# Kernel optimization log

Measured on AMD Instinct MI355X. Metric: run time of the kernel, lower is better.

Reference implementation:

```python
import jax, jax.numpy as jnp
import numpy as np

D_MODEL = 1024
NUM_HEADS = 16
D_K = D_MODEL // NUM_HEADS


def setup_inputs() -> dict:
    key = jax.random.key(0)
    k1, k2, k3, k4 = jax.random.split(key, 4)
    scale = 1.0 / np.sqrt(D_MODEL)
    inp = {
        "input": jax.random.normal(k1, (2, 2048, D_MODEL), dtype=jnp.float32),
        "W_qkv": jax.random.normal(k2, (D_MODEL, 3 * D_MODEL), dtype=jnp.float32) * scale,
        "b_qkv": jax.random.normal(k3, (3 * D_MODEL,), dtype=jnp.float32) * 0.02,
        "W_out": jax.random.normal(k4, (D_MODEL, D_MODEL), dtype=jnp.float32) * scale,
    }
    return inp


def reference(input, W_qkv, b_qkv, W_out):
    B, S, _ = input.shape
    qkv = input @ W_qkv + b_qkv                      # [B,S,3D]
    q, k, v = jnp.split(qkv, 3, axis=-1)             # each [B,S,D]
    def heads(x):
        return x.reshape(B, S, NUM_HEADS, D_K).transpose(0, 2, 1, 3)  # [B,H,S,dk]
    q, k, v = heads(q), heads(k), heads(v)
    scores = jnp.einsum("bhsd,bhtd->bhst", q, k) / jnp.sqrt(jnp.float32(D_K))
    attn = jax.nn.softmax(scores, axis=-1)           # [B,H,S,S]
    out = jnp.einsum("bhst,bhtd->bhsd", attn, v)     # [B,H,S,dk]
    out = out.transpose(0, 2, 1, 3).reshape(B, S, D_MODEL)
    return out @ W_out
```

## Files before the change

kernel.cpp:

```cpp
#include <hip/hip_runtime.h>

typedef unsigned short u16;
typedef unsigned int u32;
typedef __attribute__((ext_vector_type(8))) short short8;
typedef __attribute__((ext_vector_type(8))) __bf16 bf16x8;
typedef __attribute__((ext_vector_type(4))) float f32x4;
typedef __attribute__((ext_vector_type(16))) float f32x16;

__device__ __forceinline__ u16 f2bf(float f) {
  union { float f; u32 u; } c; c.f = f;
  u32 u = c.u + 0x7fffu + ((c.u >> 16) & 1u);
  return (u16)(u >> 16);
}
__device__ __forceinline__ f32x4 mfma16(short8 a, short8 b, f32x4 c) {
  return __builtin_amdgcn_mfma_f32_16x16x32_bf16(
      __builtin_bit_cast(bf16x8, a), __builtin_bit_cast(bf16x8, b), c, 0, 0, 0);
}
__device__ __forceinline__ f32x16 mfma32(short8 a, short8 b, f32x16 c) {
  return __builtin_amdgcn_mfma_f32_32x32x16_bf16(
      __builtin_bit_cast(bf16x8, a), __builtin_bit_cast(bf16x8, b), c, 0, 0, 0);
}
__device__ __forceinline__ float fexp2(float x) {
  float r; asm("v_exp_f32 %0, %1" : "=v"(r) : "v"(x)); return r;
}

__global__ __launch_bounds__(256) void transpose_f32_bf16(const float* __restrict__ in,
                                                          u16* __restrict__ out,
                                                          int R, int C) {
  __shared__ u16 tile[32][33];
  int tx = threadIdx.x & 31, ty = threadIdx.x >> 5;
  int c0 = blockIdx.x * 32, r0 = blockIdx.y * 32;
  for (int i = 0; i < 32; i += 8)
    tile[ty + i][tx] = f2bf(in[(size_t)(r0 + ty + i) * C + c0 + tx]);
  __syncthreads();
  for (int i = 0; i < 32; i += 8)
    out[(size_t)(c0 + ty + i) * R + r0 + tx] = tile[tx][ty + i];
}

template <bool HAS_BIAS, bool AF32, bool OUTF32, bool ROUTE>
__global__ __launch_bounds__(256) void gemm_bt(const void* __restrict__ Av,
                                               const u16* __restrict__ BT,
                                               const float* __restrict__ bias,
                                               void* __restrict__ C0v,
                                               void* __restrict__ C1v,
                                               int M, int N, int K) {
  __shared__ __align__(16) u16 As[128 * 72];
  __shared__ __align__(16) u16 Bs[128 * 72];
  const int tid = threadIdx.x;
  const int w = tid >> 6, l = tid & 63;
  const int i16 = l & 15, q4 = l >> 4;
  const int m0 = blockIdx.y * 128, n0 = blockIdx.x * 128;
  const int wm = (w >> 1) * 64, wn = (w & 1) * 64;

  f32x4 acc[4][4] = {};

  for (int k0 = 0; k0 < K; k0 += 64) {
    __syncthreads();
    for (int i = 0; i < 4; ++i) {
      int idx = i * 256 + tid;
      int row = idx >> 3, kg = (idx & 7) * 8;
      if (AF32) {
        const float* src = (const float*)Av + (size_t)(m0 + row) * K + k0 + kg;
        float4 f0 = *(const float4*)src;
        float4 f1 = *(const float4*)(src + 4);
        short8 v;
        v[0] = (short)f2bf(f0.x); v[1] = (short)f2bf(f0.y);
        v[2] = (short)f2bf(f0.z); v[3] = (short)f2bf(f0.w);
        v[4] = (short)f2bf(f1.x); v[5] = (short)f2bf(f1.y);
        v[6] = (short)f2bf(f1.z); v[7] = (short)f2bf(f1.w);
        *(short8*)&As[row * 72 + kg] = v;
      } else {
        *(short8*)&As[row * 72 + kg] =
            *(const short8*)((const u16*)Av + (size_t)(m0 + row) * K + k0 + kg);
      }
      *(short8*)&Bs[row * 72 + kg] =
          *(const short8*)&BT[(size_t)(n0 + row) * K + k0 + kg];
    }
    __syncthreads();
    for (int ks = 0; ks < 2; ++ks) {
      short8 af[4], bfr[4];
      for (int mi = 0; mi < 4; ++mi)
        af[mi] = *(short8*)&As[(wm + mi * 16 + i16) * 72 + ks * 32 + q4 * 8];
      for (int ni = 0; ni < 4; ++ni)
        bfr[ni] = *(short8*)&Bs[(wn + ni * 16 + i16) * 72 + ks * 32 + q4 * 8];
      for (int mi = 0; mi < 4; ++mi)
        for (int ni = 0; ni < 4; ++ni)
          acc[mi][ni] = mfma16(af[mi], bfr[ni], acc[mi][ni]);
    }
  }

  u16* dstb; float* dstf = nullptr; int ldc, cb;
  if (ROUTE) {
    if (n0 < 1024) { dstb = (u16*)C0v; ldc = 1024; cb = n0; }
    else           { dstb = (u16*)C1v; ldc = 2048; cb = n0 - 1024; }
  } else {
    if (OUTF32) dstf = (float*)C0v; else dstb = (u16*)C0v;
    ldc = N; cb = n0;
  }

  for (int mi = 0; mi < 4; ++mi) {
    int row = m0 + wm + mi * 16 + q4 * 4;
    for (int ni = 0; ni < 4; ++ni) {
      int nl = wn + ni * 16 + i16;
      float b = HAS_BIAS ? bias[n0 + nl] : 0.0f;
      for (int r = 0; r < 4; ++r) {
        float v = acc[mi][ni][r] + b;
        if (!ROUTE && OUTF32)
          dstf[(size_t)(row + r) * ldc + cb + nl] = v;
        else
          dstb[(size_t)(row + r) * ldc + cb + nl] = f2bf(v);
      }
    }
  }
}

__global__ __launch_bounds__(256) void attn_flash(u16* __restrict__ Qbuf,
                                                  const u16* __restrict__ KVall) {
  constexpr float CSC = 0.18033688011112042f;
  constexpr float MC  = 96.0f * CSC;
  __shared__ __align__(16) u16 Ks[2][64 * 72];
  __shared__ __align__(16) u16 Vt[2][64 * 72];
  __shared__ float RsumB[64], RsumT[64];

  const int tid = threadIdx.x;
  const int w = tid >> 6, l = tid & 63;
  const int l31 = l & 31, hi = l >> 5;
  const int qg = w >> 1, th = w & 1;

  const int L = blockIdx.x;
  const int xcd = L & 7, rr = L >> 3;
  const int qb = rr & 31, gg = rr >> 5;
  const int g = gg * 8 + xcd;
  const int h = g & 15, bat = g >> 4;
  const int q0 = qb * 64;

  u16* Q = Qbuf + (size_t)bat * 2048 * 1024;
  const u16* KV = KVall + (size_t)bat * 2048 * 2048;

  short8 qf[4];
  {
    const u16* qrow = Q + (size_t)(q0 + qg * 32 + l31) * 1024 + h * 64 + hi * 8;
#pragma unroll
    for (int ks = 0; ks < 4; ++ks) qf[ks] = *(const short8*)(qrow + ks * 16);
  }

  const int ht = qg * 64 + l;
  const int rb = ht >> 3;
  const int vc = ht & 7;
  const int cg = vc * 8;
  const u16* Kg = KV + h * 64 + cg;
  const u16* Vg = KV + 1024 + h * 64 + cg;
  u16* KsT = Ks[th];
  u16* VtT = Vt[th];
  const int tbase = th * 1024;

  short8 sk[4], sv[4];

#define LOADS(i_) {                                                          \
    const int t0_ = tbase + (i_) * 64;                                       \
    _Pragma("unroll") for (int ii = 0; ii < 4; ++ii)                         \
      sk[ii] = *(const short8*)&Kg[(size_t)(t0_ + rb + 16 * ii) * 2048];     \
    _Pragma("unroll") for (int ii = 0; ii < 2; ++ii) {                       \
      sv[2*ii]   = *(const short8*)&Vg[(size_t)(t0_ + 2*rb + 32*ii) * 2048]; \
      sv[2*ii+1] = *(const short8*)&Vg[(size_t)(t0_ + 2*rb + 32*ii + 1) * 2048]; } }

#define WRITES() {                                                           \
    _Pragma("unroll") for (int ii = 0; ii < 4; ++ii)                         \
      *(short8*)&KsT[(rb + 16 * ii) * 72 + cg] = sk[ii];                     \
    _Pragma("unroll") for (int ii = 0; ii < 2; ++ii) {                       \
      const int rho = rb + 16 * ii;                                          \
      _Pragma("unroll") for (int j = 0; j < 8; ++j) {                        \
        u32 wv = (u32)(u16)sv[2*ii][j] | ((u32)(u16)sv[2*ii+1][j] << 16);    \
        *(u32*)&VtT[(cg + j) * 72 + ((2 * rho) ^ (vc << 3))] = wv; } } }

  f32x16 o0 = {}, o1 = {};
  float sm0 = 0.f, sm1 = 0.f, sm2 = 0.f, sm3 = 0.f;

  const int sw0 = (l31 >> 3) << 3;
  const int sw1 = ((32 + l31) >> 3) << 3;

  LOADS(0);

  for (int i = 0; i < 16; ++i) {
    __syncthreads();
    WRITES();
    const int nx = (i + 1 < 16) ? i + 1 : 15;
    LOADS(nx);
    __syncthreads();

    f32x16 st0 = {}, st1 = {};
#pragma unroll
    for (int ks = 0; ks < 4; ++ks) {
      short8 kf0 = *(short8*)&KsT[l31 * 72 + ks * 16 + hi * 8];
      short8 kf1 = *(short8*)&KsT[(32 + l31) * 72 + ks * 16 + hi * 8];
      st0 = mfma32(kf0, qf[ks], st0);
      st1 = mfma32(kf1, qf[ks], st1);
    }

    u32 W[16];
#define SOFTMAX_PACK(stt, WB) {                                             \
      float p_[16];                                                         \
      _Pragma("unroll") for (int r = 0; r < 16; ++r)                        \
          p_[r] = fexp2(__builtin_fmaf(stt[r], CSC, -MC));                  \
      _Pragma("unroll") for (int r = 0; r < 16; r += 4) {                   \
        sm0 += p_[r]; sm1 += p_[r + 1]; sm2 += p_[r + 2]; sm3 += p_[r + 3]; \
      }                                                                     \
      _Pragma("unroll") for (int m = 0; m < 4; ++m)                         \
        _Pragma("unroll") for (int s = 0; s < 2; ++s)                       \
          asm("v_cvt_pk_bf16_f32 %0, %1, %2"                                \
              : "=v"(W[(WB) + m * 2 + s])                                   \
              : "v"(p_[4 * m + 2 * s]), "v"(p_[4 * m + 2 * s + 1]));        \
    }
    SOFTMAX_PACK(st0, 0)
    SOFTMAX_PACK(st1, 8)
#undef SOFTMAX_PACK

#pragma unroll
    for (int u = 0; u < 4; ++u) {
      const int base = (u >> 1) * 8 + (u & 1) * 4;
      u32 a0 = W[base], a1 = W[base + 1], b0 = W[base + 2], b1 = W[base + 3];
      asm("v_permlane32_swap_b32 %0, %1" : "+v"(a0), "+v"(b0));
      asm("v_permlane32_swap_b32 %0, %1" : "+v"(a1), "+v"(b1));
      int4 af4;
      af4.x = (int)a0; af4.y = (int)a1; af4.z = (int)b0; af4.w = (int)b1;
      const short8 pf = __builtin_bit_cast(short8, af4);
      const int toff = u * 16 + hi * 8;
      const short8 vf0 = *(short8*)&VtT[l31 * 72 + (toff ^ sw0)];
      const short8 vf1 = *(short8*)&VtT[(32 + l31) * 72 + (toff ^ sw1)];
      o0 = mfma32(pf, vf0, o0);
      o1 = mfma32(pf, vf1, o1);
    }
  }
#undef LOADS
#undef WRITES

  float rs = (sm0 + sm1) + (sm2 + sm3);
  rs += __shfl_xor(rs, 32);
  __syncthreads();
  float* MF = (float*)&Ks[0][0];
  if (th == 1) {
    float* dst = MF + (qg * 64 + l) * 36;
    *(f32x16*)dst = o0;
    *(f32x16*)(dst + 16) = o1;
    if (hi == 0) RsumB[qg * 32 + l31] = rs;
  }
  __syncthreads();
  float rtot = 0.f;
  if (th == 0) {
    const float* src = MF + (qg * 64 + l) * 36;
    o0 += *(const f32x16*)src;
    o1 += *(const f32x16*)(src + 16);
    rtot = rs + RsumB[qg * 32 + l31];
    if (hi == 0) RsumT[qg * 32 + l31] = rtot;
  }
  __syncthreads();
  if (th == 0) {
#pragma unroll
    for (int r = 0; r < 16; ++r) {
      const int qq = (r & 3) + 8 * (r >> 2) + 4 * hi;
      const float inv = 1.0f / RsumT[qg * 32 + qq];
      u16* dst = Q + (size_t)(q0 + qg * 32 + qq) * 1024 + h * 64 + l31;
      dst[0]  = f2bf(o0[r] * inv);
      dst[32] = f2bf(o1[r] * inv);
    }
  }
}

extern "C" void kernel_launch(void* const* d_in, const int* in_sizes, int n_in,
                              void* d_out, int out_size, void* d_ws, size_t ws_size,
                              hipStream_t stream) {
  const float* X    = (const float*)d_in[0];
  const float* Wqkv = (const float*)d_in[1];
  const float* bqkv = (const float*)d_in[2];
  const float* Wout = (const float*)d_in[3];

  u16* Qbuf = (u16*)d_out;
  u16* WT1  = Qbuf + (size_t)4096 * 1024;
  u16* WT2  = WT1 + (size_t)3072 * 1024;
  u16* KV   = (u16*)d_ws;
  float* Cws = (float*)d_ws;

  transpose_f32_bf16<<<dim3(96, 32), 256, 0, stream>>>(Wqkv, WT1, 1024, 3072);
  transpose_f32_bf16<<<dim3(32, 32), 256, 0, stream>>>(Wout, WT2, 1024, 1024);

  gemm_bt<true, true, false, true><<<dim3(24, 32), 256, 0, stream>>>(
      X, WT1, bqkv, Qbuf, KV, 4096, 3072, 1024);

  attn_flash<<<dim3(1024), 256, 0, stream>>>(Qbuf, KV);

  gemm_bt<false, false, true, false><<<dim3(8, 32), 256, 0, stream>>>(
      Qbuf, WT2, nullptr, Cws, nullptr, 4096, 1024, 1024);

  hipMemcpyAsync(d_out, Cws, (size_t)4096 * 1024 * sizeof(float),
                 hipMemcpyDeviceToDevice, stream);
}
```

Baseline: 222.7 us.

## Use direct global-to-LDS loads, register prefetch of fp32 A, and XCD-aware tile swizzle

```diff
diff --git a/kernel.cpp b/kernel.cpp
--- a/kernel.cpp
+++ b/kernel.cpp
@@ -22,6 +22,11 @@
 }
 __device__ __forceinline__ float fexp2(float x) {
   float r; asm("v_exp_f32 %0, %1" : "=v"(r) : "v"(x)); return r;
+}
+__device__ __forceinline__ void gl16(const u16* g, u16* l) {
+  __builtin_amdgcn_global_load_lds(
+      (const __attribute__((address_space(1))) unsigned*)g,
+      (__attribute__((address_space(3))) unsigned*)l, 16, 0, 0);
 }
 
 __global__ __launch_bounds__(256) void transpose_f32_bf16(const float* __restrict__ in,
@@ -44,49 +49,84 @@
                                                void* __restrict__ C0v,
                                                void* __restrict__ C1v,
                                                int M, int N, int K) {
-  __shared__ __align__(16) u16 As[128 * 72];
-  __shared__ __align__(16) u16 Bs[128 * 72];
+  __shared__ __align__(16) u16 As[128 * 64];
+  __shared__ __align__(16) u16 Bs[128 * 64];
   const int tid = threadIdx.x;
   const int w = tid >> 6, l = tid & 63;
   const int i16 = l & 15, q4 = l >> 4;
-  const int m0 = blockIdx.y * 128, n0 = blockIdx.x * 128;
+
+  const int nbx = gridDim.x;
+  const int nwg = nbx * gridDim.y;
+  int f = blockIdx.y * nbx + blockIdx.x;
+  int wg = (nwg & 7) ? f : ((f & 7) * (nwg >> 3) + (f >> 3));
+  const int m0 = (wg / nbx) * 128, n0 = (wg % nbx) * 128;
   const int wm = (w >> 1) * 64, wn = (w & 1) * 64;
 
+  const int srow = l >> 3, skg = (l & 7) * 8;
+  const int arow = tid >> 3, akg = (tid & 7) * 8;
+
   f32x4 acc[4][4] = {};
+  float4 pf[4][2];
+  if (AF32) {
+#pragma unroll
+    for (int i = 0; i < 4; ++i) {
+      const float* src = (const float*)Av + (size_t)(m0 + arow + i * 32) * K + akg;
+      pf[i][0] = *(const float4*)src;
+      pf[i][1] = *(const float4*)(src + 4);
+    }
+  }
 
   for (int k0 = 0; k0 < K; k0 += 64) {
+#pragma unroll
+    for (int i = 0; i < 4; ++i) {
+      const int seg = w * 4 + i, row = seg * 8 + srow;
+      gl16(&BT[(size_t)(n0 + row) * K + k0 + skg], &Bs[seg * 512]);
+    }
+    if (AF32) {
+#pragma unroll
+      for (int i = 0; i < 4; ++i) {
+        short8 v;
+        v[0] = (short)f2bf(pf[i][0].x); v[1] = (short)f2bf(pf[i][0].y);
+        v[2] = (short)f2bf(pf[i][0].z); v[3] = (short)f2bf(pf[i][0].w);
+        v[4] = (short)f2bf(pf[i][1].x); v[5] = (short)f2bf(pf[i][1].y);
+        v[6] = (short)f2bf(pf[i][1].z); v[7] = (short)f2bf(pf[i][1].w);
+        *(short8*)&As[(arow + i * 32) * 64 + akg] = v;
+      }
+    } else {
+#pragma unroll
+      for (int i = 0; i < 4; ++i) {
+        const int seg = w * 4 + i, row = seg * 8 + srow;
+        gl16((const u16*)Av + (size_t)(m0 + row) * K + k0 + skg, &As[seg * 512]);
+      }
+    }
     __syncthreads();
-    for (int i = 0; i < 4; ++i) {
-      int idx = i * 256 + tid;
-      int row = idx >> 3, kg = (idx & 7) * 8;
-      if (AF32) {
-        const float* src = (const float*)Av + (size_t)(m0 + row) * K + k0 + kg;
-        float4 f0 = *(const float4*)src;
-        float4 f1 = *(const float4*)(src + 4);
-        short8 v;
-        v[0] = (short)f2bf(f0.x); v[1] = (short)f2bf(f0.y);
-        v[2] = (short)f2bf(f0.z); v[3] = (short)f2bf(f0.w);
-        v[4] = (short)f2bf(f1.x); v[5] = (short)f2bf(f1.y);
-        v[6] = (short)f2bf(f1.z); v[7] = (short)f2bf(f1.w);
-        *(short8*)&As[row * 72 + kg] = v;
-      } else {
-        *(short8*)&As[row * 72 + kg] =
-            *(const short8*)((const u16*)Av + (size_t)(m0 + row) * K + k0 + kg);
+
+    if (AF32 && k0 + 64 < K) {
+#pragma unroll
+      for (int i = 0; i < 4; ++i) {
+        const float* src =
+            (const float*)Av + (size_t)(m0 + arow + i * 32) * K + (k0 + 64) + akg;
+        pf[i][0] = *(const float4*)src;
+        pf[i][1] = *(const float4*)(src + 4);
       }
-      *(short8*)&Bs[row * 72 + kg] =
-          *(const short8*)&BT[(size_t)(n0 + row) * K + k0 + kg];
-    }
-    __syncthreads();
+    }
+
+#pragma unroll
     for (int ks = 0; ks < 2; ++ks) {
       short8 af[4], bfr[4];
+#pragma unroll
       for (int mi = 0; mi < 4; ++mi)
-        af[mi] = *(short8*)&As[(wm + mi * 16 + i16) * 72 + ks * 32 + q4 * 8];
+        af[mi] = *(short8*)&As[(wm + mi * 16 + i16) * 64 + ks * 32 + q4 * 8];
+#pragma unroll
       for (int ni = 0; ni < 4; ++ni)
-        bfr[ni] = *(short8*)&Bs[(wn + ni * 16 + i16) * 72 + ks * 32 + q4 * 8];
+        bfr[ni] = *(short8*)&Bs[(wn + ni * 16 + i16) * 64 + ks * 32 + q4 * 8];
+#pragma unroll
       for (int mi = 0; mi < 4; ++mi)
+#pragma unroll
         for (int ni = 0; ni < 4; ++ni)
           acc[mi][ni] = mfma16(af[mi], bfr[ni], acc[mi][ni]);
     }
+    __syncthreads();
   }
 
   u16* dstb; float* dstf = nullptr; int ldc, cb;
```

Measured after the change: 232.6 us. +4.4%, slower.
